# Kernel optimization log

Hardware: AMD Instinct MI355X
Metric: run time of the kernel (lower is better)

The kernel has to match this reference:

```python
import jax, jax.numpy as jnp
import numpy as np

B, T, H, V = 64, 128, 50, 8192  # batch, window, lstm hidden (=embedding_size=50 in source), vocab
REC_DROP, DENSE_DROP = 0.3, 0.5


def setup_inputs() -> dict:
    key = jax.random.key(0)
    ks = jax.random.split(key, 16)
    n = lambda k, *s: 0.1 * jax.random.normal(k, s, dtype=jnp.float32)
    inp = {}
    inp["batched_input"] = jax.random.randint(ks[0], (B, T), 0, V)
    inp["E"] = n(ks[1], V, H)                  # embedding table
    inp["Wx"] = n(ks[2], H, 4 * H)             # LSTM input kernel (i,f,c,o)
    inp["U"] = n(ks[3], 4, H, H)               # LSTM recurrent kernel per gate
    inp["b"] = jnp.zeros((4 * H,), jnp.float32)
    inp["W1"] = n(ks[4], H, V)                 # denseTypeOne, first application
    inp["b1"] = jnp.zeros((V,), jnp.float32)   # shared bias (layer reused)
    inp["W1b"] = n(ks[5], V, V)                # denseTypeOne, second application (V->V)
    inp["W2"] = n(ks[6], V, V)                 # denseTypeTwo (sigmoid)
    inp["b2"] = jnp.zeros((V,), jnp.float32)
    # Frozen dropout masks (inverted-dropout scaling baked in).
    inp["rec_mask"] = jax.random.bernoulli(ks[7], 1.0 - REC_DROP, (4, B, H)).astype(jnp.float32) / (1.0 - REC_DROP)
    inp["dmask1"] = jax.random.bernoulli(ks[8], 1.0 - DENSE_DROP, (B, T // 2, V)).astype(jnp.float32) / (1.0 - DENSE_DROP)
    inp["dmask2"] = jax.random.bernoulli(ks[9], 1.0 - DENSE_DROP, (B, T // 2, V)).astype(jnp.float32) / (1.0 - DENSE_DROP)
    return inp


def _lstm(emb, Wx, U, b, rec_mask):
    # emb: [B,T,H]; precompute input contribution once, scan over time.
    zx = jnp.einsum('bth,hk->tbk', emb, Wx) + b  # [T,B,4H]

    def step(carry, z_t):
        h, c = carry
        # per-gate recurrent dropout on h, as Keras does off the cuDNN path
        rec = jnp.einsum('gbh,ghk->bgk', h[None, :, :] * rec_mask, U)  # [B,4,H]
        z = z_t.reshape(B, 4, H) + rec
        i = jax.nn.sigmoid(z[:, 0])
        f = jax.nn.sigmoid(z[:, 1])
        g = jnp.tanh(z[:, 2])
        o = jax.nn.sigmoid(z[:, 3])
        c_new = f * c + i * g
        h_new = o * jnp.tanh(c_new)
        return (h_new, c_new), h_new

    init = (jnp.zeros((B, H), emb.dtype), jnp.zeros((B, H), emb.dtype))
    _, hs = jax.lax.scan(step, init, zx)  # [T,B,H]
    return jnp.transpose(hs, (1, 0, 2))   # [B,T,H]


def reference(batched_input, E, Wx, U, b, W1, b1, W1b, W2, b2, rec_mask, dmask1, dmask2):
    emb = E[batched_input]                       # [B,T,H]
    seq = _lstm(emb, Wx, U, b, rec_mask)         # [B,T,H]
    pooled = seq.reshape(B, T // 2, 2, H).max(axis=2)  # MaxPool1D(pool=2)
    d1 = jax.nn.relu(pooled @ W1 + b1)           # [B,T/2,V]
    x = d1 * dmask1                              # dropout 0.5 (training=True)
    d2 = jax.nn.relu(x @ W1b + b1)               # denseTypeOne reused (shared bias)
    x = d2 * dmask2
    prbs = jax.nn.sigmoid(x @ W2 + b2)           # [B,T/2,V]
    return prbs
```

## Files before the change

### kernel.cpp

```cpp
#include <hip/hip_runtime.h>


#define Bc 64
#define Tc 128
#define Hc 50
#define Vc 8192
#define Mrows 4096

typedef unsigned short u16;
typedef short bf16x8 __attribute__((ext_vector_type(8)));
typedef float f32x4 __attribute__((ext_vector_type(4)));

__device__ __forceinline__ u16 f2bf(float x) {
  union { float f; unsigned int u; } v; v.f = x;
  unsigned int r = v.u + 0x7fffu + ((v.u >> 16) & 1u);
  return (u16)(r >> 16);
}

__device__ __forceinline__ void async_copy16(void* lds, const void* g) {
  __builtin_amdgcn_global_load_lds(
      (const __attribute__((address_space(1))) void*)g,
      (__attribute__((address_space(3))) void*)lds, 16, 0, 0);
}

__device__ __forceinline__ float sigmoidf(float x) {
  return 1.0f / (1.0f + __expf(-x));
}

__global__ __launch_bounds__(256) void zx_kernel(
    const int* __restrict__ tok, const float* __restrict__ E,
    const float* __restrict__ Wx, const float* __restrict__ bvec,
    float* __restrict__ zx) {
  const int tb = blockIdx.x;
  const int t = tb >> 6, b = tb & 63;
  __shared__ float e_s[Hc];
  const int id = tok[b * Tc + t];
  if (threadIdx.x < Hc) e_s[threadIdx.x] = E[id * Hc + threadIdx.x];
  __syncthreads();
  if (threadIdx.x < 4 * Hc) {
    float acc = bvec[threadIdx.x];
    #pragma unroll
    for (int h = 0; h < Hc; ++h) acc += e_s[h] * Wx[h * 200 + threadIdx.x];
    zx[(size_t)tb * 200 + threadIdx.x] = acc;
  }
}

__global__ __launch_bounds__(256) void lstm_kernel(
    const float* __restrict__ zx, const float* __restrict__ U,
    const float* __restrict__ rec_mask, u16* __restrict__ pooled) {
  const int b = blockIdx.x;
  const int tid = threadIdx.x;
  __shared__ float Us[4 * Hc * Hc];
  __shared__ float recm[4 * Hc];
  __shared__ float h_s[Hc], c_s[Hc], hprev[Hc];
  __shared__ float hm[4 * Hc], z_s[4 * Hc];

  for (int i = tid; i < 4 * Hc * Hc; i += 256) Us[i] = U[i];
  if (tid < 200) recm[tid] = rec_mask[(tid / Hc) * Bc * Hc + b * Hc + (tid % Hc)];
  if (tid < Hc) { h_s[tid] = 0.f; c_s[tid] = 0.f; }
  __syncthreads();

  for (int t = 0; t < Tc; ++t) {
    if (tid < 200) hm[tid] = h_s[tid % Hc] * recm[tid];
    __syncthreads();
    if (tid < 200) {
      const int g = tid / Hc, k = tid % Hc;
      float acc = zx[((size_t)t * Bc + b) * 200 + tid];
      const float* Ug = Us + g * Hc * Hc;
      const float* hmg = hm + g * Hc;
      #pragma unroll
      for (int h = 0; h < Hc; ++h) acc += hmg[h] * Ug[h * Hc + k];
      z_s[tid] = acc;
    }
    __syncthreads();
    if (tid < Hc) {
      const int k = tid;
      const float i_ = sigmoidf(z_s[k]);
      const float f_ = sigmoidf(z_s[Hc + k]);
      const float g_ = tanhf(z_s[2 * Hc + k]);
      const float o_ = sigmoidf(z_s[3 * Hc + k]);
      const float c = f_ * c_s[k] + i_ * g_;
      const float h = o_ * tanhf(c);
      c_s[k] = c; h_s[k] = h;
      if ((t & 1) != 0) {
        pooled[((size_t)b * 64 + (t >> 1)) * 64 + k] = f2bf(fmaxf(hprev[k], h));
      } else {
        hprev[k] = h;
      }
    }
    if ((t & 1) != 0 && tid >= Hc && tid < 64)
      pooled[((size_t)b * 64 + (t >> 1)) * 64 + tid] = 0;
    __syncthreads();
  }
}

__global__ __launch_bounds__(256) void w1t_kernel(
    const float* __restrict__ W1, u16* __restrict__ W1T) {
  const int idx = blockIdx.x * 256 + threadIdx.x;
  const int n = idx >> 6, k = idx & 63;
  const float v = (k < Hc) ? W1[(size_t)k * Vc + n] : 0.f;
  W1T[idx] = f2bf(v);
}

__global__ __launch_bounds__(256) void wt_kernel(
    const float* __restrict__ W, u16* __restrict__ WT) {
  __shared__ float sm[128][65];
  const int t = threadIdx.x;
  const size_t k0 = (size_t)blockIdx.x * 128;
  const size_t n0 = (size_t)blockIdx.y * 64;
  {
    const int n = t & 63, kr = t >> 6;
    #pragma unroll
    for (int i = 0; i < 32; ++i) {
      const int k = i * 4 + kr;
      sm[k][n] = W[(k0 + k) * Vc + n0 + n];
    }
  }
  __syncthreads();
  {
    const int kk = (t & 63) * 2, nr = t >> 6;
    #pragma unroll
    for (int i = 0; i < 16; ++i) {
      const int nn = i * 4 + nr;
      ushort2 v;
      v.x = f2bf(sm[kk][nn]);
      v.y = f2bf(sm[kk + 1][nn]);
      *(ushort2*)&WT[(n0 + nn) * Vc + k0 + kk] = v;
    }
  }
}

template <bool SIGMOID>
__global__ __launch_bounds__(256, 2) void gemm_bt(
    const u16* __restrict__ A, const u16* __restrict__ Bt,
    const float* __restrict__ bias, const float* __restrict__ mask,
    void* __restrict__ Cout, const int M, const int N, const int K) {
  __shared__ u16 As[128 * 64];
  __shared__ u16 Bs[128 * 64];
  const int tid = threadIdx.x;
  const int wave = tid >> 6;
  const int lane = tid & 63;
  const int wr = (wave >> 1) << 6;
  const int wc = (wave & 1) << 6;
  const long tileM = (long)blockIdx.y * 128;
  const long tileN = (long)blockIdx.x * 128;

  const int lrow = lane >> 3;
  const int cg8 = (((lane & 7) ^ lrow) << 3);
  const u16* Ab = A + tileM * K;
  const u16* Bb = Bt + tileN * K;

  f32x4 acc[4][4] = {};

  for (int k0 = 0; k0 < K; k0 += 64) {
    #pragma unroll
    for (int q4 = 0; q4 < 4; ++q4) {
      const int r = (wave << 5) + (q4 << 3) + lrow;
      const int ldsoff = (wave * 4 + q4) << 10;
      async_copy16((char*)As + ldsoff, Ab + (long)r * K + k0 + cg8);
      async_copy16((char*)Bs + ldsoff, Bb + (long)r * K + k0 + cg8);
    }
    __syncthreads();
    #pragma unroll
    for (int kk = 0; kk < 64; kk += 32) {
      const int ch = (kk >> 3) + (lane >> 4);
      bf16x8 af[4], bf[4];
      #pragma unroll
      for (int i = 0; i < 4; ++i) {
        const int ra = wr + (i << 4) + (lane & 15);
        af[i] = *(const bf16x8*)(As + ra * 64 + ((ch ^ (ra & 7)) << 3));
      }
      #pragma unroll
      for (int j = 0; j < 4; ++j) {
        const int rb = wc + (j << 4) + (lane & 15);
        bf[j] = *(const bf16x8*)(Bs + rb * 64 + ((ch ^ (rb & 7)) << 3));
      }
      #pragma unroll
      for (int i = 0; i < 4; ++i)
        #pragma unroll
        for (int j = 0; j < 4; ++j)
          acc[i][j] = __builtin_amdgcn_mfma_f32_16x16x32_bf16(af[i], bf[j], acc[i][j], 0, 0, 0);
    }
    __syncthreads();
  }

  const int qrow = (lane >> 4) << 2;
  const int qcol = lane & 15;
  #pragma unroll
  for (int j = 0; j < 4; ++j) {
    const long col = tileN + wc + (j << 4) + qcol;
    const float bv = bias[col];
    #pragma unroll
    for (int i = 0; i < 4; ++i) {
      const long row0 = tileM + wr + (i << 4) + qrow;
      #pragma unroll
      for (int r = 0; r < 4; ++r) {
        const long off = (row0 + r) * N + col;
        const float z = acc[i][j][r] + bv;
        if constexpr (SIGMOID) {
          ((float*)Cout)[off] = sigmoidf(z);
        } else {
          ((u16*)Cout)[off] = f2bf(fmaxf(z, 0.f) * mask[off]);
        }
      }
    }
  }
}

template <bool SIGMOID>
__global__ __launch_bounds__(512, 2) void gemm256(
    const u16* __restrict__ A, const u16* __restrict__ Bt,
    const float* __restrict__ bias, const float* __restrict__ mask,
    void* __restrict__ Cout, const int M, const int N, const int K) {
  __shared__ u16 As[2][16384];
  __shared__ u16 Bs[2][16384];
  const int tid = threadIdx.x;
  const int wave = tid >> 6;
  const int lane = tid & 63;
  const int l15 = lane & 15;
  const int chb = lane >> 4;
  const int wm64 = ((wave >> 2) & 1) << 6;
  const int wn32 = (wave & 3) << 5;

  const int nwg = gridDim.x;
  const int cpx = nwg >> 3;
  const int bid = blockIdx.x;
  const int swz = (bid & 7) * cpx + (bid >> 3);
  const int ntN = N >> 8;
  const long tileM = (long)(swz / ntN) << 8;
  const long tileN = (long)(swz % ntN) << 8;

  const u16* Ab = A + tileM * K;
  const u16* Bb = Bt + tileN * K;

  const int srow = tid >> 3;
  const int schunk = ((tid & 7) ^ (srow & 7)) << 3;
  const long srowK = (long)srow * K + schunk;
  const long K64 = (long)K << 6;
  const int stgoff = wave << 10;
  const int nt = K >> 6;

  f32x4 acc[8][4] = {};

#define STG(DSTBASE, SRCB, KT, HH) do {                                   \
    const int _kt = (KT) < nt ? (KT) : nt - 1;                            \
    const u16* _s = (SRCB) + ((long)(HH) * 128) * K + srowK + ((long)_kt << 6); \
    char* _d = (char*)(DSTBASE) + (HH) * 16384 + stgoff;                  \
    async_copy16(_d, _s);                                                 \
    async_copy16(_d + 8192, _s + K64);                                    \
  } while (0)

  STG(As[0], Ab, 0, 0);
  STG(Bs[0], Bb, 0, 0);
  STG(As[0], Ab, 0, 1);
  STG(Bs[0], Bb, 0, 1);
  STG(As[1], Ab, 1, 0);
  STG(Bs[1], Bb, 1, 0);
  asm volatile("s_waitcnt vmcnt(8)" ::: "memory");
  __builtin_amdgcn_s_barrier();

#define PHASE(CUR, MH, NH, STAGE_STMT, WAIT_STMT) do {                    \
    bf16x8 af[2][4], bv[2][2];                                            \
    const u16* _A = As[CUR];                                              \
    const u16* _B = Bs[CUR];                                              \
    _Pragma("unroll")                                                     \
    for (int kc = 0; kc < 2; ++kc) {                                      \
      const int ch = (kc << 2) + chb;                                     \
      _Pragma("unroll")                                                   \
      for (int i = 0; i < 4; ++i) {                                       \
        const int ra = (MH) * 128 + wm64 + (i << 4) + l15;                \
        af[kc][i] = *(const bf16x8*)(_A + ra * 64 + ((ch ^ (ra & 7)) << 3)); \
      }                                                                   \
      _Pragma("unroll")                                                   \
      for (int j = 0; j < 2; ++j) {                                       \
        const int rb = (NH) * 128 + wn32 + (j << 4) + l15;                \
        bv[kc][j] = *(const bf16x8*)(_B + rb * 64 + ((ch ^ (rb & 7)) << 3)); \
      }                                                                   \
    }                                                                     \
    STAGE_STMT;                                                           \
    __builtin_amdgcn_s_barrier();                                         \
    asm volatile("s_waitcnt lgkmcnt(0)" ::: "memory");                    \
    __builtin_amdgcn_sched_barrier(0);                                    \
    __builtin_amdgcn_s_setprio(1);                                        \
    _Pragma("unroll")                                                     \
    for (int kc = 0; kc < 2; ++kc)                                        \
      _Pragma("unroll")                                                   \
      for (int i = 0; i < 4; ++i)                                         \
        _Pragma("unroll")                                                 \
        for (int j = 0; j < 2; ++j)                                       \
          acc[(MH) * 4 + i][(NH) * 2 + j] =                               \
              __builtin_amdgcn_mfma_f32_16x16x32_bf16(                    \
                  af[kc][i], bv[kc][j], acc[(MH) * 4 + i][(NH) * 2 + j],  \
                  0, 0, 0);                                               \
    __builtin_amdgcn_s_setprio(0);                                        \
    WAIT_STMT;                                                            \
    __builtin_amdgcn_s_barrier();                                         \
  } while (0)

  for (int T = 0; T < nt; T += 2) {
    PHASE(0, 0, 0, STG(As[1], Ab, T + 1, 1),
          asm volatile("s_waitcnt vmcnt(6)" ::: "memory"));
    PHASE(0, 0, 1, STG(Bs[1], Bb, T + 1, 1), (void)0);
    PHASE(0, 1, 0, STG(As[0], Ab, T + 2, 0), (void)0);
    PHASE(0, 1, 1, STG(Bs[0], Bb, T + 2, 0),
          asm volatile("s_waitcnt vmcnt(8)" ::: "memory"));
    PHASE(1, 0, 0, STG(As[0], Ab, T + 2, 1),
          asm volatile("s_waitcnt vmcnt(6)" ::: "memory"));
    PHASE(1, 0, 1, STG(Bs[0], Bb, T + 2, 1), (void)0);
    PHASE(1, 1, 0, STG(As[1], Ab, T + 3, 0), (void)0);
    PHASE(1, 1, 1, STG(Bs[1], Bb, T + 3, 0),
          asm volatile("s_waitcnt vmcnt(8)" ::: "memory"));
  }

#undef PHASE
#undef STG

  const int qrow = (lane >> 4) << 2;
  #pragma unroll
  for (int nh = 0; nh < 2; ++nh) {
    #pragma unroll
    for (int j = 0; j < 2; ++j) {
      const long col = tileN + nh * 128 + wn32 + (j << 4) + l15;
      const float bvv = bias[col];
      #pragma unroll
      for (int mh = 0; mh < 2; ++mh) {
        #pragma unroll
        for (int i = 0; i < 4; ++i) {
          const long row0 = tileM + mh * 128 + wm64 + (i << 4) + qrow;
          #pragma unroll
          for (int r = 0; r < 4; ++r) {
            const long off = (row0 + r) * N + col;
            const float z = acc[mh * 4 + i][nh * 2 + j][r] + bvv;
            if constexpr (SIGMOID) {
              ((float*)Cout)[off] = sigmoidf(z);
            } else {
              ((u16*)Cout)[off] = f2bf(fmaxf(z, 0.f) * mask[off]);
            }
          }
        }
      }
    }
  }
}

extern "C" void kernel_launch(void* const* d_in, const int* in_sizes, int n_in,
                              void* d_out, int out_size, void* d_ws, size_t ws_size,
                              hipStream_t stream) {
  const int*   tok  = (const int*)  d_in[0];
  const float* E    = (const float*)d_in[1];
  const float* Wx   = (const float*)d_in[2];
  const float* U    = (const float*)d_in[3];
  const float* bvec = (const float*)d_in[4];
  const float* W1   = (const float*)d_in[5];
  const float* b1   = (const float*)d_in[6];
  const float* W1b  = (const float*)d_in[7];
  const float* W2   = (const float*)d_in[8];
  const float* b2   = (const float*)d_in[9];
  const float* recm = (const float*)d_in[10];
  const float* dm1  = (const float*)d_in[11];
  const float* dm2  = (const float*)d_in[12];
  float* out = (float*)d_out;

  char* w = (char*)d_ws;
  u16* Wt     = (u16*)w;  w += (size_t)Vc * Vc * 2;
  u16* A1     = (u16*)w;  w += (size_t)Mrows * Vc * 2;
  u16* A2     = (u16*)w;  w += (size_t)Mrows * Vc * 2;
  u16* W1T    = (u16*)w;  w += (size_t)Vc * 64 * 2;
  u16* pooled = (u16*)w;  w += (size_t)Mrows * 64 * 2;
  float* zx   = (float*)w;

  zx_kernel  <<<Bc * Tc, 256, 0, stream>>>(tok, E, Wx, bvec, zx);
  lstm_kernel<<<Bc, 256, 0, stream>>>(zx, U, recm, pooled);
  w1t_kernel <<<(Vc * 64) / 256, 256, 0, stream>>>(W1, W1T);
  gemm_bt<false><<<dim3(Vc / 128, Mrows / 128), 256, 0, stream>>>(
      pooled, W1T, b1, dm1, A1, Mrows, Vc, 64);
  wt_kernel<<<dim3(Vc / 128, Vc / 64), 256, 0, stream>>>(W1b, Wt);
  gemm256<false><<<dim3((Mrows / 256) * (Vc / 256)), 512, 0, stream>>>(
      A1, Wt, b1, dm2, A2, Mrows, Vc, Vc);
  wt_kernel<<<dim3(Vc / 128, Vc / 64), 256, 0, stream>>>(W2, Wt);
  gemm256<true><<<dim3((Mrows / 256) * (Vc / 256)), 512, 0, stream>>>(
      A2, Wt, b2, nullptr, out, Mrows, Vc, Vc);
}
```

Measured before the change: 2.283 ms.

## Restructure GEMM main loop to reuse B fragments across M halves

Replaces the four independent phases per K-tile with a TILE4 schedule that keeps two sets of B fragments in registers (bv0, bv1) and reuses them across both M halves. Each K-tile needs fewer LDS reads, and the global-to-LDS staging is reordered so that a whole buffer's next tile is issued in stages during compute. The prologue now prefetches both full tiles. The cost is more live registers and a more fragile hand-tuned vmcnt and barrier schedule, which risks lower occupancy or a race on buffer reuse.

```diff
diff --git a/kernel.cpp b/kernel.cpp
--- a/kernel.cpp
+++ b/kernel.cpp
@@ -241,6 +241,7 @@
   const int nt = K >> 6;
 
   f32x4 acc[8][4] = {};
+  bf16x8 af[2][4], bv0[2][2], bv1[2][2];
 
 #define STG(DSTBASE, SRCB, KT, HH) do {                                   \
     const int _kt = (KT) < nt ? (KT) : nt - 1;                            \
@@ -250,19 +251,8 @@
     async_copy16(_d + 8192, _s + K64);                                    \
   } while (0)
 
-  STG(As[0], Ab, 0, 0);
-  STG(Bs[0], Bb, 0, 0);
-  STG(As[0], Ab, 0, 1);
-  STG(Bs[0], Bb, 0, 1);
-  STG(As[1], Ab, 1, 0);
-  STG(Bs[1], Bb, 1, 0);
-  asm volatile("s_waitcnt vmcnt(8)" ::: "memory");
-  __builtin_amdgcn_s_barrier();
-
-#define PHASE(CUR, MH, NH, STAGE_STMT, WAIT_STMT) do {                    \
-    bf16x8 af[2][4], bv[2][2];                                            \
+#define LDA(CUR, MH) do {                                                 \
     const u16* _A = As[CUR];                                              \
-    const u16* _B = Bs[CUR];                                              \
     _Pragma("unroll")                                                     \
     for (int kc = 0; kc < 2; ++kc) {                                      \
       const int ch = (kc << 2) + chb;                                     \
@@ -271,16 +261,23 @@
         const int ra = (MH) * 128 + wm64 + (i << 4) + l15;                \
         af[kc][i] = *(const bf16x8*)(_A + ra * 64 + ((ch ^ (ra & 7)) << 3)); \
       }                                                                   \
+    }                                                                     \
+  } while (0)
+
+#define LDB(CUR, NH, BV) do {                                             \
+    const u16* _B = Bs[CUR];                                              \
+    _Pragma("unroll")                                                     \
+    for (int kc = 0; kc < 2; ++kc) {                                      \
+      const int ch = (kc << 2) + chb;                                     \
       _Pragma("unroll")                                                   \
       for (int j = 0; j < 2; ++j) {                                       \
         const int rb = (NH) * 128 + wn32 + (j << 4) + l15;                \
-        bv[kc][j] = *(const bf16x8*)(_B + rb * 64 + ((ch ^ (rb & 7)) << 3)); \
+        BV[kc][j] = *(const bf16x8*)(_B + rb * 64 + ((ch ^ (rb & 7)) << 3)); \
       }                                                                   \
     }                                                                     \
-    STAGE_STMT;                                                           \
-    __builtin_amdgcn_s_barrier();                                         \
-    asm volatile("s_waitcnt lgkmcnt(0)" ::: "memory");                    \
-    __builtin_amdgcn_sched_barrier(0);                                    \
+  } while (0)
+
+#define MM(MH, NB, BV) do {                                               \
     __builtin_amdgcn_s_setprio(1);                                        \
     _Pragma("unroll")                                                     \
     for (int kc = 0; kc < 2; ++kc)                                        \
@@ -288,31 +285,72 @@
       for (int i = 0; i < 4; ++i)                                         \
         _Pragma("unroll")                                                 \
         for (int j = 0; j < 2; ++j)                                       \
-          acc[(MH) * 4 + i][(NH) * 2 + j] =                               \
+          acc[(MH) * 4 + i][(NB) + j] =                                   \
               __builtin_amdgcn_mfma_f32_16x16x32_bf16(                    \
-                  af[kc][i], bv[kc][j], acc[(MH) * 4 + i][(NH) * 2 + j],  \
+                  af[kc][i], BV[kc][j], acc[(MH) * 4 + i][(NB) + j],      \
                   0, 0, 0);                                               \
     __builtin_amdgcn_s_setprio(0);                                        \
-    WAIT_STMT;                                                            \
-    __builtin_amdgcn_s_barrier();                                         \
+  } while (0)
+
+#define BAR() __builtin_amdgcn_s_barrier()
+#define WLG0() do {                                                       \
+    asm volatile("s_waitcnt lgkmcnt(0)" ::: "memory");                    \
+    __builtin_amdgcn_sched_barrier(0);                                    \
+  } while (0)
+
+  STG(As[0], Ab, 0, 0);
+  STG(Bs[0], Bb, 0, 0);
+  STG(Bs[0], Bb, 0, 1);
+  STG(As[0], Ab, 0, 1);
+  STG(As[1], Ab, 1, 0);
+  STG(Bs[1], Bb, 1, 0);
+  STG(Bs[1], Bb, 1, 1);
+  STG(As[1], Ab, 1, 1);
+  asm volatile("s_waitcnt vmcnt(8)" ::: "memory");
+  BAR();
+
+#define TILE4(CUR, TNEXT) do {                                            \
+                                                \
+    LDA(CUR, 0);                                                          \
+    LDB(CUR, 0, bv0);                                                     \
+    asm volatile("s_waitcnt lgkmcnt(8)" ::: "memory");                    \
+    BAR(); WLG0();                                                        \
+    MM(0, 0, bv0);                                                        \
+    BAR();                                                                \
+                                    \
+    LDB(CUR, 1, bv1);                                                     \
+    STG(As[CUR], Ab, TNEXT, 0);                                           \
+    BAR(); WLG0();                                                        \
+    MM(0, 2, bv1);                                                        \
+    asm volatile("s_waitcnt vmcnt(10)" ::: "memory");                     \
+    BAR();                                                                \
+                                 \
+    LDA(CUR, 1);                                                          \
+    STG(Bs[CUR], Bb, TNEXT, 0);                                           \
+    STG(Bs[CUR], Bb, TNEXT, 1);                                           \
+    BAR(); WLG0();                                                        \
+    MM(1, 2, bv1);                                                        \
+    BAR();                                                                \
+                                  \
+    STG(As[CUR], Ab, TNEXT, 1);                                           \
+    BAR();                                                                \
+    __builtin_amdgcn_sched_barrier(0);                                    \
+    MM(1, 0, bv0);                                                        \
+    asm volatile("s_waitcnt vmcnt(10)" ::: "memory");                     \
+    BAR();                                                                \
   } while (0)
 
   for (int T = 0; T < nt; T += 2) {
-    PHASE(0, 0, 0, STG(As[1], Ab, T + 1, 1),
-          asm volatile("s_waitcnt vmcnt(6)" ::: "memory"));
-    PHASE(0, 0, 1, STG(Bs[1], Bb, T + 1, 1), (void)0);
-    PHASE(0, 1, 0, STG(As[0], Ab, T + 2, 0), (void)0);
-    PHASE(0, 1, 1, STG(Bs[0], Bb, T + 2, 0),
-          asm volatile("s_waitcnt vmcnt(8)" ::: "memory"));
-    PHASE(1, 0, 0, STG(As[0], Ab, T + 2, 1),
-          asm volatile("s_waitcnt vmcnt(6)" ::: "memory"));
-    PHASE(1, 0, 1, STG(Bs[0], Bb, T + 2, 1), (void)0);
-    PHASE(1, 1, 0, STG(As[1], Ab, T + 3, 0), (void)0);
-    PHASE(1, 1, 1, STG(Bs[1], Bb, T + 3, 0),
-          asm volatile("s_waitcnt vmcnt(8)" ::: "memory"));
-  }
-
-#undef PHASE
+    TILE4(0, T + 2);
+    TILE4(1, T + 3);
+  }
+
+#undef TILE4
+#undef WLG0
+#undef BAR
+#undef MM
+#undef LDB
+#undef LDA
 #undef STG
 
   const int qrow = (lane >> 4) << 2;
```

New measurement: 2.171 ms. -4.9%, faster.
